# Kernel optimization log

Hardware: AMD Instinct MI355X
Metric: run time of the kernel (lower is better)

The kernel has to match this reference:

```python
import jax, jax.numpy as jnp
import numpy as np

# --- NAVAR dims (from init_kwargs) ---
ND, NS, NV, HID = 2, 4, 12, 16      # n_datasets, n_samples, n_variables, hidden_dim
GROUPS = ND * NS * NV               # 96 independent grouped-conv streams
K = 4                               # kernel_size
NBLOCKS = 3                         # dilated blocks, dilations 1,2,4
B, T = 8, 2048                      # batch, sequence length


def causal_conv(x, w, b, dilation, groups):
    """Grouped causal dilated 1D conv. x:(B,C,T), w:(O, C//groups, K), b:(O,)."""
    pad = (w.shape[-1] - 1) * dilation
    y = jax.lax.conv_general_dilated(
        x, w, window_strides=(1,), padding=[(pad, 0)],
        rhs_dilation=(dilation,),
        dimension_numbers=("NCH", "OIH", "NCH"),
        feature_group_count=groups,
    )
    return y + b[None, :, None]


def setup_inputs() -> dict:
    key = jax.random.key(0)
    ks = jax.random.split(key, 5)
    s = lambda fan_in: np.float32(1.0 / np.sqrt(fan_in))
    x = jax.random.normal(ks[0], (B, ND, NS, NV, T), dtype=jnp.float32)
    # grouped input conv: 1 -> HID channels per group
    w_in = jax.random.normal(ks[1], (GROUPS * HID, 1, K), dtype=jnp.float32) * s(K)
    b_in = jnp.zeros((GROUPS * HID,), jnp.float32)
    # dilated hidden blocks: HID -> HID per group
    w_h = jax.random.normal(ks[2], (NBLOCKS, GROUPS * HID, HID, K), dtype=jnp.float32) * s(HID * K)
    b_h = jnp.zeros((NBLOCKS, GROUPS * HID), jnp.float32)
    # grouped 1x1 output conv: HID -> NV contributions per group
    w_out = jax.random.normal(ks[3], (GROUPS * NV, HID, 1), dtype=jnp.float32) * s(HID)
    b_out = jnp.zeros((GROUPS * NV,), jnp.float32)
    # NAVAR additive biases (init 0.01 as in torch code)
    biases = jnp.full((1, ND, NS, NV, 1), 0.01, jnp.float32)
    return dict(x=x, w_in=w_in, b_in=b_in, w_h=w_h, b_h=b_h,
                w_out=w_out, b_out=b_out, biases=biases)


def reference(x, w_in, b_in, w_h, b_h, w_out, b_out, biases):
    batch = x.shape[0]
    h = x.reshape(batch, GROUPS, T)                       # (B, groups, T)
    h = jax.nn.relu(causal_conv(h, w_in, b_in, 1, GROUPS))
    for i in range(NBLOCKS):                              # fixed small loop over layers
        h = jax.nn.relu(causal_conv(h, w_h[i], b_h[i], 2 ** i, GROUPS))
    c = causal_conv(h, w_out, b_out, 1, GROUPS)           # (B, groups*NV, T)
    c = c.reshape(batch, ND, NS, NV, NV, T)               # (B, nd, ns, src, dst, T)
    prediction = c.sum(axis=-3) + biases                  # sum over source variables
    contributions = jnp.swapaxes(c, -2, -3)               # (B, nd, ns, dst, src, T)
    return prediction, contributions
```

## Files before the change

kernel.cpp:

```cpp
#include <hip/hip_runtime.h>

#define T_LEN   2048
#define BATCH   8
#define HIDDEN  16
#define KSZ     4
#define NVAR    12
#define NGROUPS 96
#define TILE_OUT 232
#define BUF     256
#define HALO    24
#define NTILES  9
#define PAD     16
#define NROWS   (BUF + PAD)
#define ROWCH   24

#define NWH  (3 * NGROUPS * HIDDEN * HIDDEN * KSZ)
#define NWO  (NGROUPS * HIDDEN * 32)

typedef __attribute__((ext_vector_type(8))) short bf16x8;
typedef __attribute__((ext_vector_type(4))) float f32x4;

__device__ __forceinline__ unsigned short f2bf(float x) {
    union { float f; unsigned u; } v; v.f = x;
    unsigned r = v.u + 0x7FFFu + ((v.u >> 16) & 1u);
    return (unsigned short)(r >> 16);
}

__device__ __forceinline__ unsigned cvtpk(float lo, float hi) {
    unsigned r;
    asm("v_cvt_pk_bf16_f32 %0, %1, %2" : "=v"(r) : "v"(lo), "v"(hi));
    return r;
}

__global__ __launch_bounds__(256) void navar_pack(
        const float* __restrict__ w_h, const float* __restrict__ w_out,
        unsigned short* __restrict__ wp, unsigned short* __restrict__ wpo) {
    const int e = blockIdx.x * 256 + threadIdx.x;
    if (e < NWH) {
        const int k  = e & 63, row = e >> 6;
        const int kk = k >> 4, i = k & 15;
        wp[e] = f2bf(w_h[(row << 6) + i * 4 + kk]);
    } else {
        const int e2 = e - NWH;
        const int k = e2 & 31, m = (e2 >> 5) & 15, g = e2 >> 9;
        wpo[e2] = (k < 16 && m < 12) ? f2bf(w_out[(g * NVAR + m) * HIDDEN + k])
                                     : (unsigned short)0;
    }
}

template<int D>
__device__ __forceinline__ void mfma_layer(
        const unsigned short (*__restrict__ src)[ROWCH],
        unsigned short (*__restrict__ dst)[ROWCH],
        const bf16x8 a0, const bf16x8 a1, const f32x4 bias,
        int tile, int wv, int q, int c) {
    const int ch = (q & 1) * 8;
    const int d0 = (3 - (q >> 1)) * D;
    const int d1 = (1 - (q >> 1)) * D;

    #pragma unroll
    for (int tt = 0; tt < 4; ++tt) {
        const int pos = (wv * 4 + tt) * 16 + c;
        const bf16x8 b0 = *(const bf16x8*)&src[PAD + pos - d0][ch];
        const bf16x8 b1 = *(const bf16x8*)&src[PAD + pos - d1][ch];
        f32x4 acc = bias;
        acc = __builtin_amdgcn_mfma_f32_16x16x32_bf16(a0, b0, acc, 0, 0, 0);
        acc = __builtin_amdgcn_mfma_f32_16x16x32_bf16(a1, b1, acc, 0, 0, 0);
        const int tgp = tile * TILE_OUT + pos - HALO;
        uint2 pku;
        pku.x = cvtpk(fmaxf(acc[0], 0.f), fmaxf(acc[1], 0.f));
        pku.y = cvtpk(fmaxf(acc[2], 0.f), fmaxf(acc[3], 0.f));
        if (tgp < 0) { pku.x = 0u; pku.y = 0u; }
        *(uint2*)&dst[PAD + pos][q * 4] = pku;
    }
}

__global__ __launch_bounds__(256, 6) void navar_main(
        const float* __restrict__ x,
        const float* __restrict__ w_in,  const float* __restrict__ b_in,
        const unsigned short* __restrict__ wp, const float* __restrict__ b_h,
        const unsigned short* __restrict__ wpo, const float* __restrict__ b_out,
        float* __restrict__ contrib) {
    __shared__ unsigned short hb[2][NROWS][ROWCH];
    float* xs = (float*)&hb[1][0][0];

    const int p    = threadIdx.x;
    const int tile = blockIdx.x % NTILES;
    const int sg   = blockIdx.x / NTILES;
    const int b    = sg / NGROUPS;
    const int g    = sg % NGROUPS;
    const int tg   = tile * TILE_OUT + p - HALO;

    const int wv = p >> 6, q = (p >> 4) & 3, c = p & 15;

    const size_t wstep = (size_t)NGROUPS * HIDDEN * (HIDDEN * KSZ);
    const unsigned short* wr0 =
        wp + (size_t)(g * HIDDEN + c) * (HIDDEN * KSZ);
    bf16x8 A0[3], A1[3]; f32x4 BH[3];
    #pragma unroll
    for (int l = 0; l < 3; ++l) {
        A0[l] = *(const bf16x8*)(wr0 + l * wstep + q * 8);
        A1[l] = *(const bf16x8*)(wr0 + l * wstep + 32 + q * 8);
        BH[l] = *(const f32x4*)(b_h + (l * NGROUPS + g) * HIDDEN + q * 4);
    }
    const unsigned short* wrowo = wpo + (size_t)(g * HIDDEN + c) * 32;
    const bf16x8 AO = *(const bf16x8*)(wrowo + q * 8);
    f32x4 BO = {0.f, 0.f, 0.f, 0.f};
    if (q < 3) BO = *(const f32x4*)(b_out + g * NVAR + q * 4);

    float xv = 0.f;
    if (tg >= 0 && tg < T_LEN) xv = x[(size_t)(b * NGROUPS + g) * T_LEN + tg];
    xs[p] = xv;
    __syncthreads();

    if (p >= 3) {
        const float t0 = xs[p-3], t1 = xs[p-2], t2 = xs[p-1], t3 = xs[p];
        const float* w  = w_in + g * HIDDEN * KSZ;
        const float* bb = b_in + g * HIDDEN;
        unsigned pk[8];
        #pragma unroll
        for (int o = 0; o < HIDDEN; o += 2) {
            float e0 = fmaf(w[o*4+0], t0, bb[o]);
            e0 = fmaf(w[o*4+1], t1, e0);
            e0 = fmaf(w[o*4+2], t2, e0);
            e0 = fmaf(w[o*4+3], t3, e0);
            float e1 = fmaf(w[o*4+4], t0, bb[o+1]);
            e1 = fmaf(w[o*4+5], t1, e1);
            e1 = fmaf(w[o*4+6], t2, e1);
            e1 = fmaf(w[o*4+7], t3, e1);
            const unsigned u = cvtpk(fmaxf(e0, 0.f), fmaxf(e1, 0.f));
            pk[o >> 1] = (tg >= 0) ? u : 0u;
        }
        uint4* row = (uint4*)&hb[0][PAD + p][0];
        row[0] = make_uint4(pk[0], pk[1], pk[2], pk[3]);
        row[1] = make_uint4(pk[4], pk[5], pk[6], pk[7]);
    }
    __syncthreads();

    mfma_layer<1>(hb[0], hb[1], A0[0], A1[0], BH[0], tile, wv, q, c);
    __syncthreads();
    mfma_layer<2>(hb[1], hb[0], A0[1], A1[1], BH[1], tile, wv, q, c);
    __syncthreads();
    mfma_layer<4>(hb[0], hb[1], A0[2], A1[2], BH[2], tile, wv, q, c);
    __syncthreads();

    {
        const int gds = g / NVAR, srcv = g % NVAR;
        #pragma unroll
        for (int tt = 0; tt < 4; ++tt) {
            const int pos = (wv * 4 + tt) * 16 + c;
            const bf16x8 b0 = *(const bf16x8*)&hb[1][PAD + pos][(q & 1) * 8];
            f32x4 acc = BO;
            acc = __builtin_amdgcn_mfma_f32_16x16x32_bf16(AO, b0, acc, 0, 0, 0);
            const int tgp = tile * TILE_OUT + pos - HALO;
            if (q < 3 && pos >= HALO && tgp < T_LEN) {
                const size_t base =
                    (((size_t)b * NGROUPS + gds * NVAR) * NVAR + srcv) * T_LEN + tgp;
                #pragma unroll
                for (int r = 0; r < 4; ++r)
                    contrib[base + (size_t)(q * 4 + r) * NVAR * T_LEN] = acc[r];
            }
        }
    }
}

__global__ __launch_bounds__(256) void navar_pred(
        const float* __restrict__ contrib, const float* __restrict__ biases,
        float* __restrict__ pred) {
    const int e = (blockIdx.x * 256 + threadIdx.x) * 4;
    const int t = e % T_LEN;
    const int G = e / T_LEN;
    const float4* c = (const float4*)(contrib + (size_t)G * NVAR * T_LEN + t);
    const float bias = biases[G % NGROUPS];
    float4 acc = make_float4(bias, bias, bias, bias);
    #pragma unroll
    for (int s = 0; s < NVAR; ++s) {
        float4 v = c[(size_t)s * (T_LEN / 4)];
        acc.x += v.x; acc.y += v.y; acc.z += v.z; acc.w += v.w;
    }
    *(float4*)(pred + e) = acc;
}

extern "C" void kernel_launch(void* const* d_in, const int* in_sizes, int n_in,
                              void* d_out, int out_size, void* d_ws, size_t ws_size,
                              hipStream_t stream) {
    const float* x      = (const float*)d_in[0];
    const float* w_in   = (const float*)d_in[1];
    const float* b_in   = (const float*)d_in[2];
    const float* w_h    = (const float*)d_in[3];
    const float* b_h    = (const float*)d_in[4];
    const float* w_out  = (const float*)d_in[5];
    const float* b_out  = (const float*)d_in[6];
    const float* biases = (const float*)d_in[7];

    float* pred    = (float*)d_out;
    float* contrib = pred + (size_t)BATCH * NGROUPS * T_LEN;
    unsigned short* wp  = (unsigned short*)d_ws;
    unsigned short* wpo = wp + NWH;

    navar_pack<<<(NWH + NWO) / 256, 256, 0, stream>>>(w_h, w_out, wp, wpo);
    navar_main<<<BATCH * NGROUPS * NTILES, 256, 0, stream>>>(
        x, w_in, b_in, wp, b_h, wpo, b_out, contrib);
    navar_pred<<<(BATCH * NGROUPS * T_LEN) / (256 * 4), 256, 0, stream>>>(
        contrib, biases, pred);
}
```

Measured before the change: 145.0 us.

## Give each wave an independent time window to drop block barriers

Each wave now handles its own 64-position window (40 outputs plus a 24-sample halo) with a private LDS double buffer. This replaces block-wide __syncthreads with per-wave s_waitcnt fences, and the input taps are gathered through lane shuffles instead of a shared staging array. The cost is more halo recomputation: 24 of every 64 positions are redundant instead of 24 of 256. Block count rises from 9 to 13 tiles per stream, and the occupancy hint drops to 5.

```diff
diff --git a/kernel.cpp b/kernel.cpp
--- a/kernel.cpp
+++ b/kernel.cpp
@@ -6,13 +6,15 @@
 #define KSZ     4
 #define NVAR    12
 #define NGROUPS 96
-#define TILE_OUT 232
-#define BUF     256
-#define HALO    24
-#define NTILES  9
-#define PAD     16
-#define NROWS   (BUF + PAD)
-#define ROWCH   24
+
+#define WOUT  40
+#define WHALO 24
+#define WPOS  64
+#define WPAD  16
+#define WROWS (WPOS + WPAD)
+#define ROWCH 24
+#define NTW   52
+#define NBT   13
 
 #define NWH  (3 * NGROUPS * HIDDEN * HIDDEN * KSZ)
 #define NWO  (NGROUPS * HIDDEN * 32)
@@ -30,6 +32,11 @@
     unsigned r;
     asm("v_cvt_pk_bf16_f32 %0, %1, %2" : "=v"(r) : "v"(lo), "v"(hi));
     return r;
+}
+
+__device__ __forceinline__ void lds_fence() {
+    asm volatile("s_waitcnt lgkmcnt(0)" ::: "memory");
+    __builtin_amdgcn_sched_barrier(0);
 }
 
 __global__ __launch_bounds__(256) void navar_pack(
@@ -53,45 +60,48 @@
         const unsigned short (*__restrict__ src)[ROWCH],
         unsigned short (*__restrict__ dst)[ROWCH],
         const bf16x8 a0, const bf16x8 a1, const f32x4 bias,
-        int tile, int wv, int q, int c) {
+        int W0, int q, int c) {
     const int ch = (q & 1) * 8;
     const int d0 = (3 - (q >> 1)) * D;
     const int d1 = (1 - (q >> 1)) * D;
 
     #pragma unroll
     for (int tt = 0; tt < 4; ++tt) {
-        const int pos = (wv * 4 + tt) * 16 + c;
-        const bf16x8 b0 = *(const bf16x8*)&src[PAD + pos - d0][ch];
-        const bf16x8 b1 = *(const bf16x8*)&src[PAD + pos - d1][ch];
+        const int pos = tt * 16 + c;
+        const bf16x8 b0 = *(const bf16x8*)&src[WPAD + pos - d0][ch];
+        const bf16x8 b1 = *(const bf16x8*)&src[WPAD + pos - d1][ch];
         f32x4 acc = bias;
         acc = __builtin_amdgcn_mfma_f32_16x16x32_bf16(a0, b0, acc, 0, 0, 0);
         acc = __builtin_amdgcn_mfma_f32_16x16x32_bf16(a1, b1, acc, 0, 0, 0);
-        const int tgp = tile * TILE_OUT + pos - HALO;
+        const int tgp = W0 + pos - WHALO;
         uint2 pku;
         pku.x = cvtpk(fmaxf(acc[0], 0.f), fmaxf(acc[1], 0.f));
         pku.y = cvtpk(fmaxf(acc[2], 0.f), fmaxf(acc[3], 0.f));
         if (tgp < 0) { pku.x = 0u; pku.y = 0u; }
-        *(uint2*)&dst[PAD + pos][q * 4] = pku;
-    }
-}
-
-__global__ __launch_bounds__(256, 6) void navar_main(
+        *(uint2*)&dst[WPAD + pos][q * 4] = pku;
+    }
+}
+
+__global__ __launch_bounds__(256, 5) void navar_main(
         const float* __restrict__ x,
         const float* __restrict__ w_in,  const float* __restrict__ b_in,
         const unsigned short* __restrict__ wp, const float* __restrict__ b_h,
         const unsigned short* __restrict__ wpo, const float* __restrict__ b_out,
         float* __restrict__ contrib) {
-    __shared__ unsigned short hb[2][NROWS][ROWCH];
-    float* xs = (float*)&hb[1][0][0];
+    __shared__ unsigned short hb[4][2][WROWS][ROWCH];
 
     const int p    = threadIdx.x;
-    const int tile = blockIdx.x % NTILES;
-    const int sg   = blockIdx.x / NTILES;
+    const int wave = p >> 6, lane = p & 63;
+    const int q    = lane >> 4, c = lane & 15;
+    const int bt   = blockIdx.x % NBT;
+    const int sg   = blockIdx.x / NBT;
     const int b    = sg / NGROUPS;
     const int g    = sg % NGROUPS;
-    const int tg   = tile * TILE_OUT + p - HALO;
-
-    const int wv = p >> 6, q = (p >> 4) & 3, c = p & 15;
+    const int tw   = bt * 4 + wave;
+    const int W0   = tw * WOUT;
+
+    unsigned short (*h0)[ROWCH] = hb[wave][0];
+    unsigned short (*h1)[ROWCH] = hb[wave][1];
 
     const size_t wstep = (size_t)NGROUPS * HIDDEN * (HIDDEN * KSZ);
     const unsigned short* wr0 =
@@ -108,13 +118,14 @@
     f32x4 BO = {0.f, 0.f, 0.f, 0.f};
     if (q < 3) BO = *(const f32x4*)(b_out + g * NVAR + q * 4);
 
-    float xv = 0.f;
-    if (tg >= 0 && tg < T_LEN) xv = x[(size_t)(b * NGROUPS + g) * T_LEN + tg];
-    xs[p] = xv;
-    __syncthreads();
-
-    if (p >= 3) {
-        const float t0 = xs[p-3], t1 = xs[p-2], t2 = xs[p-1], t3 = xs[p];
+    const size_t xrow = (size_t)(b * NGROUPS + g) * T_LEN;
+    const int gx = W0 + lane - WHALO;
+    const float xv = (gx >= 0 && gx < T_LEN) ? x[xrow + gx] : 0.f;
+    const float t2 = __shfl_up(xv, 1);
+    const float t1 = __shfl_up(xv, 2);
+    const float t0 = __shfl_up(xv, 3);
+    if (lane >= 3) {
+        const float t3 = xv;
         const float* w  = w_in + g * HIDDEN * KSZ;
         const float* bb = b_in + g * HIDDEN;
         unsigned pk[8];
@@ -129,33 +140,33 @@
             e1 = fmaf(w[o*4+6], t2, e1);
             e1 = fmaf(w[o*4+7], t3, e1);
             const unsigned u = cvtpk(fmaxf(e0, 0.f), fmaxf(e1, 0.f));
-            pk[o >> 1] = (tg >= 0) ? u : 0u;
+            pk[o >> 1] = (gx >= 0) ? u : 0u;
         }
-        uint4* row = (uint4*)&hb[0][PAD + p][0];
+        uint4* row = (uint4*)&h0[WPAD + lane][0];
         row[0] = make_uint4(pk[0], pk[1], pk[2], pk[3]);
         row[1] = make_uint4(pk[4], pk[5], pk[6], pk[7]);
     }
-    __syncthreads();
-
-    mfma_layer<1>(hb[0], hb[1], A0[0], A1[0], BH[0], tile, wv, q, c);
-    __syncthreads();
-    mfma_layer<2>(hb[1], hb[0], A0[1], A1[1], BH[1], tile, wv, q, c);
-    __syncthreads();
-    mfma_layer<4>(hb[0], hb[1], A0[2], A1[2], BH[2], tile, wv, q, c);
-    __syncthreads();
+    lds_fence();
+
+    mfma_layer<1>(h0, h1, A0[0], A1[0], BH[0], W0, q, c);
+    lds_fence();
+    mfma_layer<2>(h1, h0, A0[1], A1[1], BH[1], W0, q, c);
+    lds_fence();
+    mfma_layer<4>(h0, h1, A0[2], A1[2], BH[2], W0, q, c);
+    lds_fence();
 
     {
         const int gds = g / NVAR, srcv = g % NVAR;
         #pragma unroll
         for (int tt = 0; tt < 4; ++tt) {
-            const int pos = (wv * 4 + tt) * 16 + c;
-            const bf16x8 b0 = *(const bf16x8*)&hb[1][PAD + pos][(q & 1) * 8];
+            const int pos = tt * 16 + c;
+            const bf16x8 b0 = *(const bf16x8*)&h1[WPAD + pos][(q & 1) * 8];
             f32x4 acc = BO;
             acc = __builtin_amdgcn_mfma_f32_16x16x32_bf16(AO, b0, acc, 0, 0, 0);
-            const int tgp = tile * TILE_OUT + pos - HALO;
-            if (q < 3 && pos >= HALO && tgp < T_LEN) {
+            const int t = W0 + pos - WHALO;
+            if (q < 3 && pos >= WHALO && t < T_LEN) {
                 const size_t base =
-                    (((size_t)b * NGROUPS + gds * NVAR) * NVAR + srcv) * T_LEN + tgp;
+                    (((size_t)b * NGROUPS + gds * NVAR) * NVAR + srcv) * T_LEN + t;
                 #pragma unroll
                 for (int r = 0; r < 4; ++r)
                     contrib[base + (size_t)(q * 4 + r) * NVAR * T_LEN] = acc[r];
@@ -199,7 +210,7 @@
     unsigned short* wpo = wp + NWH;
 
     navar_pack<<<(NWH + NWO) / 256, 256, 0, stream>>>(w_h, w_out, wp, wpo);
-    navar_main<<<BATCH * NGROUPS * NTILES, 256, 0, stream>>>(
+    navar_main<<<BATCH * NGROUPS * NBT, 256, 0, stream>>>(
         x, w_in, b_in, wp, b_h, wpo, b_out, contrib);
     navar_pred<<<(BATCH * NGROUPS * T_LEN) / (256 * 4), 256, 0, stream>>>(
         contrib, biases, pred);
```

Result: slower. 151.4 us (+4.4%).
